# Kernel optimization log

Measured on AMD Instinct MI355X. Metric: run time of the kernel, lower is better.

The kernel has to match this reference:

```python
import jax, jax.numpy as jnp
import numpy as np

NUM_GRAPHS = 512


def setup_inputs() -> dict:
    key = jax.random.key(0)
    ks = jax.random.split(key, 12)
    N, E, D, H, C = 100000, 1600000, 128, 128, 10
    x = jax.random.normal(ks[0], (N, D), dtype=jnp.float32)
    edge_index = jax.random.randint(ks[1], (2, E), 0, N, dtype=jnp.int64)
    batch = jnp.sort(jax.random.randint(ks[2], (N,), 0, NUM_GRAPHS, dtype=jnp.int64))
    def glorot(k, fan_in, fan_out):
        s = jnp.sqrt(6.0 / (fan_in + fan_out))
        return jax.random.uniform(k, (fan_in, fan_out), jnp.float32, -s, s)
    return {
        "x": x, "edge_index": edge_index, "batch": batch,
        "W_init": glorot(ks[3], D, H), "b_init": jnp.zeros((H,), jnp.float32),
        "W_h0": glorot(ks[4], H, H), "b_h0": jnp.zeros((H,), jnp.float32),
        "W_h1": glorot(ks[5], H, H), "b_h1": jnp.zeros((H,), jnp.float32),
        "W_out": glorot(ks[6], H, C), "b_out": jnp.zeros((C,), jnp.float32),
    }


def reference(x, edge_index, batch, W_init, b_init, W_h0, b_h0, W_h1, b_h1, W_out, b_out):
    N = x.shape[0]
    loop = jnp.arange(N, dtype=edge_index.dtype)
    # add self-loops (PyG GCNConv default)
    row = jnp.concatenate([edge_index[0], loop])  # source
    col = jnp.concatenate([edge_index[1], loop])  # target
    # symmetric normalization D^-1/2 (A+I) D^-1/2, degrees on target index
    deg = jax.ops.segment_sum(jnp.ones_like(col, dtype=x.dtype), col, num_segments=N)
    dis = jnp.where(deg > 0, jax.lax.rsqrt(jnp.maximum(deg, 1e-12)), 0.0)
    norm = dis[row] * dis[col]  # [E+N]

    def gcn_conv(h, W, b):
        h = h @ W                                    # linear first (as in PyG)
        msg = h[row] * norm[:, None]                 # gather + scale
        return jax.ops.segment_sum(msg, col, num_segments=N) + b  # scatter-add

    h = jax.nn.relu(gcn_conv(x, W_init, b_init))
    h = jax.nn.relu(gcn_conv(h, W_h0, b_h0))
    h = jax.nn.relu(gcn_conv(h, W_h1, b_h1))
    h = gcn_conv(h, W_out, b_out)
    # global mean pooling over graphs
    sums = jax.ops.segment_sum(h, batch, num_segments=NUM_GRAPHS)
    cnt = jax.ops.segment_sum(jnp.ones((N, 1), h.dtype), batch, num_segments=NUM_GRAPHS)
    return sums / jnp.maximum(cnt, 1.0)
```

## Files before the change

kernel.cpp:

```cpp
#include <hip/hip_runtime.h>


#define SCAN_BLOCKS 64
#define SCAN_THREADS (SCAN_BLOCKS * 256)

typedef unsigned short u16;
typedef unsigned int   u32;
typedef __attribute__((ext_vector_type(8))) short bf16x8;
typedef __attribute__((ext_vector_type(4))) float f32x4;

static __device__ __forceinline__ u16 f2bf(float x) {
    u32 u = __float_as_uint(x);
    u32 r = (u + 0x7fffu + ((u >> 16) & 1u)) >> 16;
    return (u16)r;
}
static __device__ __forceinline__ float bf_lo(u32 p) { return __uint_as_float(p << 16); }
static __device__ __forceinline__ float bf_hi(u32 p) { return __uint_as_float(p & 0xffff0000u); }
static __device__ __forceinline__ float bf1(u16 h) { return __uint_as_float((u32)h << 16); }

__global__ __launch_bounds__(256) void k_count(const int* __restrict__ col, int E,
                                               int* __restrict__ cnt,
                                               u16* __restrict__ rank) {
    int e = blockIdx.x * 256 + threadIdx.x;
    if (e < E) rank[e] = (u16)atomicAdd(&cnt[col[e]], 1);
}

__global__ __launch_bounds__(256) void k_scan1(const int* __restrict__ cnt,
                                               int* __restrict__ tsum, int N) {
    int t = blockIdx.x * 256 + threadIdx.x;
    int strip = (N + SCAN_THREADS - 1) / SCAN_THREADS;
    int s0 = t * strip;
    int s1 = s0 + strip; if (s1 > N) s1 = N;
    int s = 0;
    for (int i = s0; i < s1; ++i) s += (cnt[i] + 3) & ~3;
    tsum[t] = s;
}

__global__ __launch_bounds__(1024) void k_scan2(int* __restrict__ tsum) {
    __shared__ int part[1024];
    int t = threadIdx.x;
    int base = t * 16;
    int local[16];
    int s = 0;
    #pragma unroll
    for (int i = 0; i < 16; ++i) { local[i] = tsum[base + i]; s += local[i]; }
    part[t] = s;
    __syncthreads();
    for (int off = 1; off < 1024; off <<= 1) {
        int v = part[t];
        int add = (t >= off) ? part[t - off] : 0;
        __syncthreads();
        part[t] = v + add;
        __syncthreads();
    }
    int run = (t == 0) ? 0 : part[t - 1];
    #pragma unroll
    for (int i = 0; i < 16; ++i) { int c = local[i]; tsum[base + i] = run; run += c; }
}

__global__ __launch_bounds__(256) void k_scan3(const int* __restrict__ cnt,
                                               const int* __restrict__ tsum,
                                               int* __restrict__ rowptr,
                                               float* __restrict__ dis,
                                               int* __restrict__ csr, int N) {
    int t = blockIdx.x * 256 + threadIdx.x;
    int strip = (N + SCAN_THREADS - 1) / SCAN_THREADS;
    int s0 = t * strip;
    int s1 = s0 + strip; if (s1 > N) s1 = N;
    int run = tsum[t];
    for (int i = s0; i < s1; ++i) {
        int c = cnt[i];
        int r = (c + 3) & ~3;
        rowptr[i] = run;
        for (int p = run + c; p < run + r; ++p) csr[p] = N;
        run += r;
        dis[i] = rsqrtf((float)(c + 1));
    }
    if (t == SCAN_THREADS - 1) rowptr[N] = run;
}

__global__ __launch_bounds__(256) void k_fill(const int* __restrict__ row,
                                              const int* __restrict__ col, int E,
                                              const int* __restrict__ rowptr,
                                              const u16* __restrict__ rank,
                                              int* __restrict__ csr) {
    int e = blockIdx.x * 256 + threadIdx.x;
    if (e < E) {
        int c = col[e];
        csr[rowptr[c] + (int)rank[e]] = row[e];
    }
}

__global__ __launch_bounds__(256) void k_cast(const float* __restrict__ src,
                                              const float* __restrict__ dis,
                                              u16* __restrict__ bX,
                                              u16* __restrict__ bA,
                                              u16* __restrict__ bB, int N) {
    int i = blockIdx.x * 256 + threadIdx.x;
    int total = (N + 1) * 32;
    if (i >= total) return;
    int v = i >> 5;
    if (v < N) {
        float dv = dis[v];
        float4 val = ((const float4*)src)[i];
        ushort4 o;
        o.x = f2bf(dv * val.x); o.y = f2bf(dv * val.y);
        o.z = f2bf(dv * val.z); o.w = f2bf(dv * val.w);
        ((ushort4*)bX)[i] = o;
    } else {
        ushort4 z = {0, 0, 0, 0};
        ((ushort4*)bX)[i] = z;
        ((ushort4*)bA)[i] = z;
        ((ushort4*)bB)[i] = z;
    }
}

__global__ __launch_bounds__(256) void k_wprep3(const float* __restrict__ W0,
                                                const float* __restrict__ W1,
                                                const float* __restrict__ W2,
                                                u32* __restrict__ whi,
                                                u32* __restrict__ wlo) {
    int which = blockIdx.x >> 3;
    const float* W = (which == 0) ? W0 : (which == 1) ? W1 : W2;
    int t = (blockIdx.x & 7) * 256 + threadIdx.x;
    int lane = t & 63;
    int nk = t >> 6;
    int k0 = nk & 3;
    int ntile = nk >> 2;
    int n = ntile * 16 + (lane & 15);
    int kbase = k0 * 32 + (lane >> 4) * 8;
    u32 hi[4], lo[4];
    #pragma unroll
    for (int tt = 0; tt < 4; ++tt) {
        float w0 = W[(kbase + 2 * tt) * 128 + n];
        float w1 = W[(kbase + 2 * tt + 1) * 128 + n];
        u16 h0 = f2bf(w0), h1 = f2bf(w1);
        u16 l0 = f2bf(w0 - __uint_as_float((u32)h0 << 16));
        u16 l1 = f2bf(w1 - __uint_as_float((u32)h1 << 16));
        hi[tt] = (u32)h0 | ((u32)h1 << 16);
        lo[tt] = (u32)l0 | ((u32)l1 << 16);
    }
    uint4 qh = {hi[0], hi[1], hi[2], hi[3]};
    uint4 ql = {lo[0], lo[1], lo[2], lo[3]};
    int base = which * 2048;
    ((uint4*)whi)[base + t] = qh;
    ((uint4*)wlo)[base + t] = ql;
}

__global__ __launch_bounds__(256) void k_fused(const u16* __restrict__ hin,
                                               const u32* __restrict__ whi,
                                               const u32* __restrict__ wlo,
                                               const float* __restrict__ bias,
                                               u16* __restrict__ hout,
                                               const int* __restrict__ rowptr,
                                               const int* __restrict__ csr,
                                               const float* __restrict__ dis,
                                               int N, int scale_out,
                                               int proj,
                                               const float* __restrict__ Wout,
                                               float* __restrict__ tmpC, int C) {
    __shared__ u32 sS[32 * 65];
    __shared__ float dS[32];
    int tid = threadIdx.x;
    int wave = tid >> 6;
    int lane = tid & 63;
    int row0 = blockIdx.x * 32;
    const u32* hin32 = (const u32*)hin;
    const int4* csr4 = (const int4*)csr;

    for (int j = 0; j < 8; j += 2) {
        int va = row0 + wave * 8 + j;
        int vb = va + 1;
        bool hA = va < N, hB = vb < N;
        float ax = 0.f, ay = 0.f, bx = 0.f, by = 0.f;
        int ia = 0, ea = 0, ib = 0, eb = 0;
        float dva = 1.f, dvb = 1.f;
        if (hA) {
            u32 p = hin32[((u32)va << 6) + lane];
            ax = bf_lo(p); ay = bf_hi(p);
            ia = rowptr[va]; ea = rowptr[va + 1];
            dva = dis[va];
        }
        if (hB) {
            u32 p = hin32[((u32)vb << 6) + lane];
            bx = bf_lo(p); by = bf_hi(p);
            ib = rowptr[vb]; eb = rowptr[vb + 1];
            dvb = dis[vb];
        }
        while ((ia + 8 <= ea) & (ib + 8 <= eb)) {
            int4 a0 = csr4[(u32)ia >> 2];
            int4 a1 = csr4[((u32)ia >> 2) + 1];
            int4 b0 = csr4[(u32)ib >> 2];
            int4 b1 = csr4[((u32)ib >> 2) + 1];
            u32 pa0 = hin32[((u32)a0.x << 6) + lane];
            u32 pa1 = hin32[((u32)a0.y << 6) + lane];
            u32 pa2 = hin32[((u32)a0.z << 6) + lane];
            u32 pa3 = hin32[((u32)a0.w << 6) + lane];
            u32 pa4 = hin32[((u32)a1.x << 6) + lane];
            u32 pa5 = hin32[((u32)a1.y << 6) + lane];
            u32 pa6 = hin32[((u32)a1.z << 6) + lane];
            u32 pa7 = hin32[((u32)a1.w << 6) + lane];
            u32 pb0 = hin32[((u32)b0.x << 6) + lane];
            u32 pb1 = hin32[((u32)b0.y << 6) + lane];
            u32 pb2 = hin32[((u32)b0.z << 6) + lane];
            u32 pb3 = hin32[((u32)b0.w << 6) + lane];
            u32 pb4 = hin32[((u32)b1.x << 6) + lane];
            u32 pb5 = hin32[((u32)b1.y << 6) + lane];
            u32 pb6 = hin32[((u32)b1.z << 6) + lane];
            u32 pb7 = hin32[((u32)b1.w << 6) + lane];
            ax += bf_lo(pa0) + bf_lo(pa1) + bf_lo(pa2) + bf_lo(pa3);
            ay += bf_hi(pa0) + bf_hi(pa1) + bf_hi(pa2) + bf_hi(pa3);
            ax += bf_lo(pa4) + bf_lo(pa5) + bf_lo(pa6) + bf_lo(pa7);
            ay += bf_hi(pa4) + bf_hi(pa5) + bf_hi(pa6) + bf_hi(pa7);
            bx += bf_lo(pb0) + bf_lo(pb1) + bf_lo(pb2) + bf_lo(pb3);
            by += bf_hi(pb0) + bf_hi(pb1) + bf_hi(pb2) + bf_hi(pb3);
            bx += bf_lo(pb4) + bf_lo(pb5) + bf_lo(pb6) + bf_lo(pb7);
            by += bf_hi(pb4) + bf_hi(pb5) + bf_hi(pb6) + bf_hi(pb7);
            ia += 8; ib += 8;
        }
        while (ia + 8 <= ea) {
            int4 a0 = csr4[(u32)ia >> 2];
            int4 a1 = csr4[((u32)ia >> 2) + 1];
            u32 p0 = hin32[((u32)a0.x << 6) + lane];
            u32 p1 = hin32[((u32)a0.y << 6) + lane];
            u32 p2 = hin32[((u32)a0.z << 6) + lane];
            u32 p3 = hin32[((u32)a0.w << 6) + lane];
            u32 p4 = hin32[((u32)a1.x << 6) + lane];
            u32 p5 = hin32[((u32)a1.y << 6) + lane];
            u32 p6 = hin32[((u32)a1.z << 6) + lane];
            u32 p7 = hin32[((u32)a1.w << 6) + lane];
            ax += bf_lo(p0) + bf_lo(p1) + bf_lo(p2) + bf_lo(p3);
            ay += bf_hi(p0) + bf_hi(p1) + bf_hi(p2) + bf_hi(p3);
            ax += bf_lo(p4) + bf_lo(p5) + bf_lo(p6) + bf_lo(p7);
            ay += bf_hi(p4) + bf_hi(p5) + bf_hi(p6) + bf_hi(p7);
            ia += 8;
        }
        if (ia < ea) {
            int4 a0 = csr4[(u32)ia >> 2];
            u32 p0 = hin32[((u32)a0.x << 6) + lane];
            u32 p1 = hin32[((u32)a0.y << 6) + lane];
            u32 p2 = hin32[((u32)a0.z << 6) + lane];
            u32 p3 = hin32[((u32)a0.w << 6) + lane];
            ax += bf_lo(p0) + bf_lo(p1) + bf_lo(p2) + bf_lo(p3);
            ay += bf_hi(p0) + bf_hi(p1) + bf_hi(p2) + bf_hi(p3);
        }
        while (ib + 8 <= eb) {
            int4 b0 = csr4[(u32)ib >> 2];
            int4 b1 = csr4[((u32)ib >> 2) + 1];
            u32 p0 = hin32[((u32)b0.x << 6) + lane];
            u32 p1 = hin32[((u32)b0.y << 6) + lane];
            u32 p2 = hin32[((u32)b0.z << 6) + lane];
            u32 p3 = hin32[((u32)b0.w << 6) + lane];
            u32 p4 = hin32[((u32)b1.x << 6) + lane];
            u32 p5 = hin32[((u32)b1.y << 6) + lane];
            u32 p6 = hin32[((u32)b1.z << 6) + lane];
            u32 p7 = hin32[((u32)b1.w << 6) + lane];
            bx += bf_lo(p0) + bf_lo(p1) + bf_lo(p2) + bf_lo(p3);
            by += bf_hi(p0) + bf_hi(p1) + bf_hi(p2) + bf_hi(p3);
            bx += bf_lo(p4) + bf_lo(p5) + bf_lo(p6) + bf_lo(p7);
            by += bf_hi(p4) + bf_hi(p5) + bf_hi(p6) + bf_hi(p7);
            ib += 8;
        }
        if (ib < eb) {
            int4 b0 = csr4[(u32)ib >> 2];
            u32 p0 = hin32[((u32)b0.x << 6) + lane];
            u32 p1 = hin32[((u32)b0.y << 6) + lane];
            u32 p2 = hin32[((u32)b0.z << 6) + lane];
            u32 p3 = hin32[((u32)b0.w << 6) + lane];
            bx += bf_lo(p0) + bf_lo(p1) + bf_lo(p2) + bf_lo(p3);
            by += bf_hi(p0) + bf_hi(p1) + bf_hi(p2) + bf_hi(p3);
        }
        if (hA) {
            sS[(wave * 8 + j) * 65 + lane] =
                (u32)f2bf(dva * ax) | ((u32)f2bf(dva * ay) << 16);
            if (lane == 0) dS[wave * 8 + j] = dva;
        }
        if (hB) {
            sS[(wave * 8 + j + 1) * 65 + lane] =
                (u32)f2bf(dvb * bx) | ((u32)f2bf(dvb * by) << 16);
            if (lane == 0) dS[wave * 8 + j + 1] = dvb;
        }
    }
    __syncthreads();

    f32x4 acc[2][2] = {{{0.f,0.f,0.f,0.f},{0.f,0.f,0.f,0.f}},
                       {{0.f,0.f,0.f,0.f},{0.f,0.f,0.f,0.f}}};
    int mA = lane & 15;
    int qA = lane >> 4;
    #pragma unroll
    for (int k0 = 0; k0 < 4; ++k0) {
        union { u32 u[4]; bf16x8 v; } A0, A1;
        int ub = k0 * 16 + qA * 4;
        #pragma unroll
        for (int tt = 0; tt < 4; ++tt) {
            A0.u[tt] = sS[mA * 65 + ub + tt];
            A1.u[tt] = sS[(mA + 16) * 65 + ub + tt];
        }
        #pragma unroll
        for (int ct = 0; ct < 2; ++ct) {
            int ntk = ((2 * wave + ct) * 4 + k0) * 64 + lane;
            union { uint4 q; bf16x8 v; } BH, BL;
            BH.q = ((const uint4*)whi)[ntk];
            BL.q = ((const uint4*)wlo)[ntk];
            acc[0][ct] = __builtin_amdgcn_mfma_f32_16x16x32_bf16(A0.v, BH.v, acc[0][ct], 0, 0, 0);
            acc[0][ct] = __builtin_amdgcn_mfma_f32_16x16x32_bf16(A0.v, BL.v, acc[0][ct], 0, 0, 0);
            acc[1][ct] = __builtin_amdgcn_mfma_f32_16x16x32_bf16(A1.v, BH.v, acc[1][ct], 0, 0, 0);
            acc[1][ct] = __builtin_amdgcn_mfma_f32_16x16x32_bf16(A1.v, BL.v, acc[1][ct], 0, 0, 0);
        }
    }

    if (!proj) {
        #pragma unroll
        for (int rt = 0; rt < 2; ++rt) {
            #pragma unroll
            for (int ct = 0; ct < 2; ++ct) {
                int col = (2 * wave + ct) * 16 + (lane & 15);
                float bb = bias[col];
                #pragma unroll
                for (int r = 0; r < 4; ++r) {
                    int rloc = rt * 16 + (lane >> 4) * 4 + r;
                    int row = row0 + rloc;
                    if (row < N) {
                        float o = fmaxf(acc[rt][ct][r] + bb, 0.f);
                        if (scale_out) o *= dS[rloc];
                        hout[((u32)row << 7) + col] = f2bf(o);
                    }
                }
            }
        }
    } else {
        __syncthreads();
        u16* hS16 = (u16*)sS;
        #pragma unroll
        for (int rt = 0; rt < 2; ++rt) {
            #pragma unroll
            for (int ct = 0; ct < 2; ++ct) {
                int col = (2 * wave + ct) * 16 + (lane & 15);
                float bb = bias[col];
                #pragma unroll
                for (int r = 0; r < 4; ++r) {
                    int rloc = rt * 16 + (lane >> 4) * 4 + r;
                    hS16[rloc * 130 + col] = f2bf(fmaxf(acc[rt][ct][r] + bb, 0.f));
                }
            }
        }
        __syncthreads();
        int c = tid & 15;
        int rl = tid >> 4;
        #pragma unroll
        for (int half = 0; half < 2; ++half) {
            int rr = rl + 16 * half;
            int row = row0 + rr;
            if (row < N) {
                float a2 = 0.f;
                if (c < C) {
                    #pragma unroll 8
                    for (int k = 0; k < 128; ++k)
                        a2 += bf1(hS16[rr * 130 + k]) * Wout[k * C + c];
                    a2 *= dS[rr];
                }
                tmpC[((u32)row << 4) + c] = a2;
            }
        }
        if (blockIdx.x == 0 && tid < 16) tmpC[((u32)N << 4) + tid] = 0.f;
    }
}

__global__ __launch_bounds__(256) void k_aggout(const float* __restrict__ tp,
                                                const int* __restrict__ rowptr,
                                                const int* __restrict__ csr,
                                                const float* __restrict__ dis,
                                                float* __restrict__ node,
                                                int N) {
    int tid = threadIdx.x;
    int wave = tid >> 6;
    int lane = tid & 63;
    int g = lane >> 4;
    int c = lane & 15;
    int v = blockIdx.x * 16 + wave * 4 + g;
    if (v >= N) return;
    const int4* csr4 = (const int4*)csr;
    float acc = tp[((u32)v << 4) + c];
    int i = rowptr[v], e = rowptr[v + 1];
    for (; i + 8 <= e; i += 8) {
        int4 q0 = csr4[(u32)i >> 2];
        int4 q1 = csr4[((u32)i >> 2) + 1];
        float p0 = tp[((u32)q0.x << 4) + c];
        float p1 = tp[((u32)q0.y << 4) + c];
        float p2 = tp[((u32)q0.z << 4) + c];
        float p3 = tp[((u32)q0.w << 4) + c];
        float p4 = tp[((u32)q1.x << 4) + c];
        float p5 = tp[((u32)q1.y << 4) + c];
        float p6 = tp[((u32)q1.z << 4) + c];
        float p7 = tp[((u32)q1.w << 4) + c];
        acc += p0 + p1 + p2 + p3 + p4 + p5 + p6 + p7;
    }
    if (i < e) {
        int4 q0 = csr4[(u32)i >> 2];
        float p0 = tp[((u32)q0.x << 4) + c];
        float p1 = tp[((u32)q0.y << 4) + c];
        float p2 = tp[((u32)q0.z << 4) + c];
        float p3 = tp[((u32)q0.w << 4) + c];
        acc += p0 + p1 + p2 + p3;
    }
    node[((u32)v << 4) + c] = dis[v] * acc;
}

__global__ __launch_bounds__(256) void k_pool(const float* __restrict__ node,
                                              const int* __restrict__ batch,
                                              const float* __restrict__ bout,
                                              float* __restrict__ out,
                                              int N, int C) {
    __shared__ float red[256];
    int g = blockIdx.x;
    int tid = threadIdx.x;
    int c = tid & 15;
    int rg = tid >> 4;
    int lo = 0, hi = N;
    while (lo < hi) { int m = (lo + hi) >> 1; if (batch[m] < g) lo = m + 1; else hi = m; }
    int lb = lo;
    hi = N;
    while (lo < hi) { int m = (lo + hi) >> 1; if (batch[m] <= g) lo = m + 1; else hi = m; }
    int ub = lo;
    float acc = 0.f;
    for (int v = lb + rg; v < ub; v += 16)
        acc += node[((u32)v << 4) + c];
    red[tid] = acc;
    __syncthreads();
    #pragma unroll
    for (int s = 8; s >= 1; s >>= 1) {
        if (rg < s) red[tid] += red[tid + s * 16];
        __syncthreads();
    }
    if (tid < C) {
        float cnt = (float)(ub - lb);
        out[g * C + tid] = (red[tid] + cnt * bout[tid]) / fmaxf(cnt, 1.0f);
    }
}

extern "C" void kernel_launch(void* const* d_in, const int* in_sizes, int n_in,
                              void* d_out, int out_size, void* d_ws, size_t ws_size,
                              hipStream_t stream) {
    const float* x      = (const float*)d_in[0];
    const int*   ei     = (const int*)d_in[1];
    const int*   batch  = (const int*)d_in[2];
    const float* W_init = (const float*)d_in[3];
    const float* b_init = (const float*)d_in[4];
    const float* W_h0   = (const float*)d_in[5];
    const float* b_h0   = (const float*)d_in[6];
    const float* W_h1   = (const float*)d_in[7];
    const float* b_h1   = (const float*)d_in[8];
    const float* W_out  = (const float*)d_in[9];
    const float* b_out  = (const float*)d_in[10];

    int N = in_sizes[0] / 128;
    int E = in_sizes[1] / 2;
    int C = in_sizes[10];
    int G = out_size / C;

    size_t off = 0;
    auto alloc = [&](size_t bytes) -> char* {
        char* p = (char*)d_ws + off;
        off += (bytes + 255) & ~(size_t)255;
        return p;
    };
    u16*   bufX   = (u16*)  alloc((size_t)(N + 1) * 128 * 2);
    u16*   bufA   = (u16*)  alloc((size_t)(N + 1) * 128 * 2);
    u16*   bufB   = (u16*)  alloc((size_t)(N + 1) * 128 * 2);
    float* dis    = (float*)alloc((size_t)N * 4);
    int*   rowptr = (int*)  alloc((size_t)(N + 1) * 4);
    int*   csr    = (int*)  alloc(((size_t)E + 3 * (size_t)N + 8) * 4);
    int*   tsum   = (int*)  alloc((size_t)SCAN_THREADS * 4);
    u32*   whi    = (u32*)  alloc(3 * 2048 * 16);
    u32*   wlo    = (u32*)  alloc(3 * 2048 * 16);
    size_t zoff   = off;
    int*   cnt    = (int*)  alloc((size_t)N * 4);
    size_t zbytes = off - zoff;

    u16*   rank   = (u16*)bufB;
    float* tmpC   = (float*)bufX;
    float* nodeP  = (float*)bufB;

    hipMemsetAsync(cnt, 0, zbytes, stream);

    const int* rowi = ei;
    const int* coli = ei + E;

    int eb = (E + 255) / 256;
    k_count<<<eb, 256, 0, stream>>>(coli, E, cnt, rank);
    k_scan1<<<SCAN_BLOCKS, 256, 0, stream>>>(cnt, tsum, N);
    k_scan2<<<1, 1024, 0, stream>>>(tsum);
    k_scan3<<<SCAN_BLOCKS, 256, 0, stream>>>(cnt, tsum, rowptr, dis, csr, N);
    k_fill<<<eb, 256, 0, stream>>>(rowi, coli, E, rowptr, rank, csr);

    k_wprep3<<<24, 256, 0, stream>>>(W_init, W_h0, W_h1, whi, wlo);

    int cg = ((N + 1) * 32 + 255) / 256;
    k_cast<<<cg, 256, 0, stream>>>(x, dis, bufX, bufA, bufB, N);

    int fb = (N + 31) / 32;
    int ob = (N + 15) / 16;

    k_fused<<<fb, 256, 0, stream>>>(bufX, whi,         wlo,         b_init, bufA, rowptr, csr, dis, N, 1, 0, nullptr, nullptr, C);
    k_fused<<<fb, 256, 0, stream>>>(bufA, whi + 8192,  wlo + 8192,  b_h0,   bufB, rowptr, csr, dis, N, 1, 0, nullptr, nullptr, C);
    k_fused<<<fb, 256, 0, stream>>>(bufB, whi + 16384, wlo + 16384, b_h1,   bufA, rowptr, csr, dis, N, 0, 1, W_out, tmpC, C);

    k_aggout <<<ob, 256, 0, stream>>>(tmpC, rowptr, csr, dis, nodeP, N);
    k_pool   <<<G, 256, 0, stream>>>(nodeP, batch, b_out, (float*)d_out, N, C);
}
```

Measured before the change: 506.1 us.

## Use MFMA for output projection and fuse final aggregation into pooling

The 128x10 output projection in the last fused layer moves from a scalar per-thread dot product to split-bf16 (hi+lo) MFMA, with W_out pre-packed alongside the other weights in the prep kernel. The final sparse aggregation is folded into the pooling kernel, so there is no separate node buffer write and reread and one fewer launch. The trade-off is that pooling now runs on only 512 blocks, each doing a whole graph's gather work, which may lower parallelism for the aggregation step.

```diff
diff --git a/kernel.cpp b/kernel.cpp
--- a/kernel.cpp
+++ b/kernel.cpp
@@ -16,7 +16,6 @@
 }
 static __device__ __forceinline__ float bf_lo(u32 p) { return __uint_as_float(p << 16); }
 static __device__ __forceinline__ float bf_hi(u32 p) { return __uint_as_float(p & 0xffff0000u); }
-static __device__ __forceinline__ float bf1(u16 h) { return __uint_as_float((u32)h << 16); }
 
 __global__ __launch_bounds__(256) void k_count(const int* __restrict__ col, int E,
                                                int* __restrict__ cnt,
@@ -115,36 +114,61 @@
     }
 }
 
-__global__ __launch_bounds__(256) void k_wprep3(const float* __restrict__ W0,
+__global__ __launch_bounds__(256) void k_wprep4(const float* __restrict__ W0,
                                                 const float* __restrict__ W1,
                                                 const float* __restrict__ W2,
+                                                const float* __restrict__ Wo,
                                                 u32* __restrict__ whi,
-                                                u32* __restrict__ wlo) {
-    int which = blockIdx.x >> 3;
-    const float* W = (which == 0) ? W0 : (which == 1) ? W1 : W2;
-    int t = (blockIdx.x & 7) * 256 + threadIdx.x;
-    int lane = t & 63;
-    int nk = t >> 6;
-    int k0 = nk & 3;
-    int ntile = nk >> 2;
-    int n = ntile * 16 + (lane & 15);
-    int kbase = k0 * 32 + (lane >> 4) * 8;
-    u32 hi[4], lo[4];
-    #pragma unroll
-    for (int tt = 0; tt < 4; ++tt) {
-        float w0 = W[(kbase + 2 * tt) * 128 + n];
-        float w1 = W[(kbase + 2 * tt + 1) * 128 + n];
-        u16 h0 = f2bf(w0), h1 = f2bf(w1);
-        u16 l0 = f2bf(w0 - __uint_as_float((u32)h0 << 16));
-        u16 l1 = f2bf(w1 - __uint_as_float((u32)h1 << 16));
-        hi[tt] = (u32)h0 | ((u32)h1 << 16);
-        lo[tt] = (u32)l0 | ((u32)l1 << 16);
-    }
-    uint4 qh = {hi[0], hi[1], hi[2], hi[3]};
-    uint4 ql = {lo[0], lo[1], lo[2], lo[3]};
-    int base = which * 2048;
-    ((uint4*)whi)[base + t] = qh;
-    ((uint4*)wlo)[base + t] = ql;
+                                                u32* __restrict__ wlo, int C) {
+    if (blockIdx.x < 24) {
+        int which = blockIdx.x >> 3;
+        const float* W = (which == 0) ? W0 : (which == 1) ? W1 : W2;
+        int t = (blockIdx.x & 7) * 256 + threadIdx.x;
+        int lane = t & 63;
+        int nk = t >> 6;
+        int k0 = nk & 3;
+        int ntile = nk >> 2;
+        int n = ntile * 16 + (lane & 15);
+        int kbase = k0 * 32 + (lane >> 4) * 8;
+        u32 hi[4], lo[4];
+        #pragma unroll
+        for (int tt = 0; tt < 4; ++tt) {
+            float w0 = W[(kbase + 2 * tt) * 128 + n];
+            float w1 = W[(kbase + 2 * tt + 1) * 128 + n];
+            u16 h0 = f2bf(w0), h1 = f2bf(w1);
+            u16 l0 = f2bf(w0 - __uint_as_float((u32)h0 << 16));
+            u16 l1 = f2bf(w1 - __uint_as_float((u32)h1 << 16));
+            hi[tt] = (u32)h0 | ((u32)h1 << 16);
+            lo[tt] = (u32)l0 | ((u32)l1 << 16);
+        }
+        uint4 qh = {hi[0], hi[1], hi[2], hi[3]};
+        uint4 ql = {lo[0], lo[1], lo[2], lo[3]};
+        int base = which * 2048;
+        ((uint4*)whi)[base + t] = qh;
+        ((uint4*)wlo)[base + t] = ql;
+    } else {
+        int t = threadIdx.x;
+        int lane = t & 63;
+        int k0 = t >> 6;
+        int n = lane & 15;
+        int kbase = k0 * 32 + (lane >> 4) * 8;
+        bool vc = (n < C);
+        u32 hi[4], lo[4];
+        #pragma unroll
+        for (int tt = 0; tt < 4; ++tt) {
+            float w0 = vc ? Wo[(kbase + 2 * tt) * C + n] : 0.f;
+            float w1 = vc ? Wo[(kbase + 2 * tt + 1) * C + n] : 0.f;
+            u16 h0 = f2bf(w0), h1 = f2bf(w1);
+            u16 l0 = f2bf(w0 - __uint_as_float((u32)h0 << 16));
+            u16 l1 = f2bf(w1 - __uint_as_float((u32)h1 << 16));
+            hi[tt] = (u32)h0 | ((u32)h1 << 16);
+            lo[tt] = (u32)l0 | ((u32)l1 << 16);
+        }
+        uint4 qh = {hi[0], hi[1], hi[2], hi[3]};
+        uint4 ql = {lo[0], lo[1], lo[2], lo[3]};
+        ((uint4*)whi)[6144 + t] = qh;
+        ((uint4*)wlo)[6144 + t] = ql;
+    }
 }
 
 __global__ __launch_bounds__(256) void k_fused(const u16* __restrict__ hin,
@@ -157,9 +181,10 @@
                                                const float* __restrict__ dis,
                                                int N, int scale_out,
                                                int proj,
-                                               const float* __restrict__ Wout,
-                                               float* __restrict__ tmpC, int C) {
-    __shared__ u32 sS[32 * 65];
+                                               const u32* __restrict__ pwhi,
+                                               const u32* __restrict__ pwlo,
+                                               float* __restrict__ tmpC) {
+    __shared__ u32 sS[32 * 68];
     __shared__ float dS[32];
     int tid = threadIdx.x;
     int wave = tid >> 6;
@@ -340,77 +365,43 @@
                 #pragma unroll
                 for (int r = 0; r < 4; ++r) {
                     int rloc = rt * 16 + (lane >> 4) * 4 + r;
-                    hS16[rloc * 130 + col] = f2bf(fmaxf(acc[rt][ct][r] + bb, 0.f));
+                    hS16[rloc * 136 + col] = f2bf(fmaxf(acc[rt][ct][r] + bb, 0.f));
                 }
             }
         }
         __syncthreads();
-        int c = tid & 15;
-        int rl = tid >> 4;
-        #pragma unroll
-        for (int half = 0; half < 2; ++half) {
-            int rr = rl + 16 * half;
-            int row = row0 + rr;
-            if (row < N) {
-                float a2 = 0.f;
-                if (c < C) {
-                    #pragma unroll 8
-                    for (int k = 0; k < 128; ++k)
-                        a2 += bf1(hS16[rr * 130 + k]) * Wout[k * C + c];
-                    a2 *= dS[rr];
-                }
-                tmpC[((u32)row << 4) + c] = a2;
+        if (wave < 2) {
+            int m = lane & 15;
+            int quad = lane >> 4;
+            f32x4 a2 = {0.f, 0.f, 0.f, 0.f};
+            #pragma unroll
+            for (int k0 = 0; k0 < 4; ++k0) {
+                bf16x8 Afrag = *(bf16x8*)&hS16[(wave * 16 + m) * 136 + k0 * 32 + quad * 8];
+                union { uint4 q; bf16x8 v; } BH, BL;
+                BH.q = ((const uint4*)pwhi)[k0 * 64 + lane];
+                BL.q = ((const uint4*)pwlo)[k0 * 64 + lane];
+                a2 = __builtin_amdgcn_mfma_f32_16x16x32_bf16(Afrag, BH.v, a2, 0, 0, 0);
+                a2 = __builtin_amdgcn_mfma_f32_16x16x32_bf16(Afrag, BL.v, a2, 0, 0, 0);
             }
+            #pragma unroll
+            for (int r = 0; r < 4; ++r) {
+                int rloc = wave * 16 + quad * 4 + r;
+                int row = row0 + rloc;
+                if (row < N) tmpC[((u32)row << 4) + m] = a2[r] * dS[rloc];
+            }
         }
         if (blockIdx.x == 0 && tid < 16) tmpC[((u32)N << 4) + tid] = 0.f;
     }
 }
 
-__global__ __launch_bounds__(256) void k_aggout(const float* __restrict__ tp,
-                                                const int* __restrict__ rowptr,
-                                                const int* __restrict__ csr,
-                                                const float* __restrict__ dis,
-                                                float* __restrict__ node,
-                                                int N) {
-    int tid = threadIdx.x;
-    int wave = tid >> 6;
-    int lane = tid & 63;
-    int g = lane >> 4;
-    int c = lane & 15;
-    int v = blockIdx.x * 16 + wave * 4 + g;
-    if (v >= N) return;
-    const int4* csr4 = (const int4*)csr;
-    float acc = tp[((u32)v << 4) + c];
-    int i = rowptr[v], e = rowptr[v + 1];
-    for (; i + 8 <= e; i += 8) {
-        int4 q0 = csr4[(u32)i >> 2];
-        int4 q1 = csr4[((u32)i >> 2) + 1];
-        float p0 = tp[((u32)q0.x << 4) + c];
-        float p1 = tp[((u32)q0.y << 4) + c];
-        float p2 = tp[((u32)q0.z << 4) + c];
-        float p3 = tp[((u32)q0.w << 4) + c];
-        float p4 = tp[((u32)q1.x << 4) + c];
-        float p5 = tp[((u32)q1.y << 4) + c];
-        float p6 = tp[((u32)q1.z << 4) + c];
-        float p7 = tp[((u32)q1.w << 4) + c];
-        acc += p0 + p1 + p2 + p3 + p4 + p5 + p6 + p7;
-    }
-    if (i < e) {
-        int4 q0 = csr4[(u32)i >> 2];
-        float p0 = tp[((u32)q0.x << 4) + c];
-        float p1 = tp[((u32)q0.y << 4) + c];
-        float p2 = tp[((u32)q0.z << 4) + c];
-        float p3 = tp[((u32)q0.w << 4) + c];
-        acc += p0 + p1 + p2 + p3;
-    }
-    node[((u32)v << 4) + c] = dis[v] * acc;
-}
-
-__global__ __launch_bounds__(256) void k_pool(const float* __restrict__ node,
-                                              const int* __restrict__ batch,
-                                              const float* __restrict__ bout,
-                                              float* __restrict__ out,
-                                              int N, int C) {
+__global__ __launch_bounds__(256) void k_aggpool(const float* __restrict__ tp,
+                                                 const int* __restrict__ rowptr,
+                                                 const int* __restrict__ csr,
+                                                 const float* __restrict__ dis,
+                                                 const int* __restrict__ batch,
+                                                 const float* __restrict__ bout,
+                                                 float* __restrict__ out,
+                                                 int N, int C) {
     __shared__ float red[256];
     int g = blockIdx.x;
     int tid = threadIdx.x;
@@ -422,10 +413,27 @@
     hi = N;
     while (lo < hi) { int m = (lo + hi) >> 1; if (batch[m] <= g) lo = m + 1; else hi = m; }
     int ub = lo;
-    float acc = 0.f;
-    for (int v = lb + rg; v < ub; v += 16)
-        acc += node[((u32)v << 4) + c];
-    red[tid] = acc;
+    const int4* csr4 = (const int4*)csr;
+    float pacc = 0.f;
+    for (int v = lb + rg; v < ub; v += 16) {
+        float acc = tp[((u32)v << 4) + c];
+        int i = rowptr[v], e = rowptr[v + 1];
+        for (; i + 8 <= e; i += 8) {
+            int4 q0 = csr4[(u32)i >> 2];
+            int4 q1 = csr4[((u32)i >> 2) + 1];
+            acc += tp[((u32)q0.x << 4) + c] + tp[((u32)q0.y << 4) + c]
+                 + tp[((u32)q0.z << 4) + c] + tp[((u32)q0.w << 4) + c]
+                 + tp[((u32)q1.x << 4) + c] + tp[((u32)q1.y << 4) + c]
+                 + tp[((u32)q1.z << 4) + c] + tp[((u32)q1.w << 4) + c];
+        }
+        if (i < e) {
+            int4 q0 = csr4[(u32)i >> 2];
+            acc += tp[((u32)q0.x << 4) + c] + tp[((u32)q0.y << 4) + c]
+                 + tp[((u32)q0.z << 4) + c] + tp[((u32)q0.w << 4) + c];
+        }
+        pacc += dis[v] * acc;
+    }
+    red[tid] = pacc;
     __syncthreads();
     #pragma unroll
     for (int s = 8; s >= 1; s >>= 1) {
@@ -471,15 +479,14 @@
     int*   rowptr = (int*)  alloc((size_t)(N + 1) * 4);
     int*   csr    = (int*)  alloc(((size_t)E + 3 * (size_t)N + 8) * 4);
     int*   tsum   = (int*)  alloc((size_t)SCAN_THREADS * 4);
-    u32*   whi    = (u32*)  alloc(3 * 2048 * 16);
-    u32*   wlo    = (u32*)  alloc(3 * 2048 * 16);
+    u32*   whi    = (u32*)  alloc((3 * 2048 + 256) * 16);
+    u32*   wlo    = (u32*)  alloc((3 * 2048 + 256) * 16);
     size_t zoff   = off;
     int*   cnt    = (int*)  alloc((size_t)N * 4);
     size_t zbytes = off - zoff;
 
     u16*   rank   = (u16*)bufB;
     float* tmpC   = (float*)bufX;
-    float* nodeP  = (float*)bufB;
 
     hipMemsetAsync(cnt, 0, zbytes, stream);
 
@@ -493,18 +500,16 @@
     k_scan3<<<SCAN_BLOCKS, 256, 0, stream>>>(cnt, tsum, rowptr, dis, csr, N);
     k_fill<<<eb, 256, 0, stream>>>(rowi, coli, E, rowptr, rank, csr);
 
-    k_wprep3<<<24, 256, 0, stream>>>(W_init, W_h0, W_h1, whi, wlo);
+    k_wprep4<<<25, 256, 0, stream>>>(W_init, W_h0, W_h1, W_out, whi, wlo, C);
 
     int cg = ((N + 1) * 32 + 255) / 256;
     k_cast<<<cg, 256, 0, stream>>>(x, dis, bufX, bufA, bufB, N);
 
     int fb = (N + 31) / 32;
-    int ob = (N + 15) / 16;
-
-    k_fused<<<fb, 256, 0, stream>>>(bufX, whi,         wlo,         b_init, bufA, rowptr, csr, dis, N, 1, 0, nullptr, nullptr, C);
-    k_fused<<<fb, 256, 0, stream>>>(bufA, whi + 8192,  wlo + 8192,  b_h0,   bufB, rowptr, csr, dis, N, 1, 0, nullptr, nullptr, C);
-    k_fused<<<fb, 256, 0, stream>>>(bufB, whi + 16384, wlo + 16384, b_h1,   bufA, rowptr, csr, dis, N, 0, 1, W_out, tmpC, C);
-
-    k_aggout <<<ob, 256, 0, stream>>>(tmpC, rowptr, csr, dis, nodeP, N);
-    k_pool   <<<G, 256, 0, stream>>>(nodeP, batch, b_out, (float*)d_out, N, C);
-}
+
+    k_fused<<<fb, 256, 0, stream>>>(bufX, whi,         wlo,         b_init, bufA, rowptr, csr, dis, N, 1, 0, nullptr, nullptr, nullptr);
+    k_fused<<<fb, 256, 0, stream>>>(bufA, whi + 8192,  wlo + 8192,  b_h0,   bufB, rowptr, csr, dis, N, 1, 0, nullptr, nullptr, nullptr);
+    k_fused<<<fb, 256, 0, stream>>>(bufB, whi + 16384, wlo + 16384, b_h1,   bufA, rowptr, csr, dis, N, 0, 1, whi + 24576, wlo + 24576, tmpC);
+
+    k_aggpool<<<G, 256, 0, stream>>>(tmpC, rowptr, csr, dis, batch, b_out, (float*)d_out, N, C);
+}
```

After: 498.4 us. No clear change (-1.5%).
